# Optimization experiments

Hardware: AMD Instinct MI355X
Metric: run time of the kernel (lower is better)

Reference implementation:

```python
import jax, jax.numpy as jnp
import numpy as np

WS = (8, 8)          # window size
NHEAD = 6
D_MODEL = 192

def _rel_pos_index(ws):
    coords = np.stack(np.meshgrid(np.arange(ws[0]), np.arange(ws[1]), indexing='ij'))  # (2, wh, ww)
    cf = coords.reshape(2, -1)                          # (2, N)
    rel = cf[:, :, None] - cf[:, None, :]               # (2, N, N)
    rel = rel.transpose(1, 2, 0).astype(np.int64)       # (N, N, 2)
    rel[:, :, 0] += ws[0] - 1
    rel[:, :, 1] += ws[1] - 1
    rel[:, :, 0] *= 2 * ws[1] - 1
    return rel.sum(-1)                                  # (N, N)

REL_IDX = jnp.asarray(_rel_pos_index(WS))

def setup_inputs() -> dict:
    key = jax.random.key(0)
    ks = jax.random.split(key, 6)
    B, H, W, C = 4, 256, 256, D_MODEL
    x = jax.random.normal(ks[0], (B, H * W, C), dtype=jnp.float32)
    qkv_w = jax.random.normal(ks[1], (3 * C, C), dtype=jnp.float32) * 0.02
    qkv_b = jnp.zeros((3 * C,), dtype=jnp.float32)
    proj_w = jax.random.normal(ks[2], (C, C), dtype=jnp.float32) * 0.02
    proj_b = jnp.zeros((C,), dtype=jnp.float32)
    n_bias = (2 * WS[0] - 1) * (2 * WS[1] - 1)
    rpb_table = jax.random.normal(ks[3], (n_bias, NHEAD), dtype=jnp.float32) * 0.02
    return {"x": x, "qkv_w": qkv_w, "qkv_b": qkv_b, "proj_w": proj_w,
            "proj_b": proj_b, "rpb_table": rpb_table, "H": H, "W": W}

def reference(x, qkv_w, qkv_b, proj_w, proj_b, rpb_table, H, W):
    B, Ni, C = x.shape
    h, d = NHEAD, C // NHEAD
    wh, ww = WS
    nH, nW = H // wh, W // ww
    N = wh * ww
    # window partition: (B, H, W, C) -> (B*nH*nW, N, C)
    xw = x.reshape(B, nH, wh, nW, ww, C).transpose(0, 1, 3, 2, 4, 5).reshape(-1, N, C)
    qkv = xw @ qkv_w.T + qkv_b                           # (B_, N, 3C)
    B_ = xw.shape[0]
    qkv = qkv.reshape(B_, N, 3, h, d).transpose(2, 0, 3, 1, 4)  # (3, B_, h, N, d)
    q, k, v = qkv[0], qkv[1], qkv[2]
    scale = d ** -0.5
    attn = jnp.einsum('bhnd,bhmd->bhnm', q, k) * scale   # (B_, h, N, N)
    bias = rpb_table[REL_IDX.reshape(-1)].reshape(N, N, h).transpose(2, 0, 1)  # (h, N, N)
    attn = jax.nn.softmax(attn + bias[None], axis=-1)
    out = jnp.einsum('bhnm,bhmd->bhnd', attn, v)         # (B_, h, N, d)
    out = out.transpose(0, 2, 1, 3).reshape(B_, N, C)
    out = out @ proj_w.T + proj_b
    # window reverse: (B*nH*nW, N, C) -> (B, H*W, C)
    out = out.reshape(B, nH, nW, wh, ww, C).transpose(0, 1, 3, 2, 4, 5).reshape(B, Ni, C)
    return out
```

## Files before the change

kernel.cpp:

```cpp
#include <hip/hip_runtime.h>

#define CDIM 192
#define NHEAD 6

typedef __bf16 bf16x8 __attribute__((ext_vector_type(8)));
typedef float f32x4 __attribute__((ext_vector_type(4)));

#define Q_OFF  0
#define K_OFF  25600
#define VT_OFF 51200
#define SMEM_BYTES 78848
#define XS  200
#define QS  200
#define KS  200
#define VTS 72
#define AOS 200
#define PS  72
#define OFS 196
#define SCALE 0.17677669529663687f

__device__ __forceinline__ unsigned short f2b(float f) {
    unsigned int u = __float_as_uint(f);
    u = (u + 0x7FFFu + ((u >> 16) & 1u)) >> 16;
    return (unsigned short)u;
}

#define WS_W1   0
#define WS_W2   221184
#define WS_BIAS 294912

__global__ void prep(const float* __restrict__ qkv_w, const float* __restrict__ proj_w,
                     const float* __restrict__ rpb,
                     unsigned short* __restrict__ W1, unsigned short* __restrict__ W2,
                     float* __restrict__ BIAS) {
    int t = blockIdx.x * 256 + threadIdx.x;
    if (t < 110592) { W1[t] = f2b(qkv_w[t]); return; }
    t -= 110592;
    if (t < 36864)  { W2[t] = f2b(proj_w[t]); return; }
    t -= 36864;
    {
        int h = t >> 12, ij = t & 4095;
        int i = ij >> 6, j = ij & 63;
        int idx = ((i >> 3) - (j >> 3) + 7) * 15 + ((i & 7) - (j & 7) + 7);
        BIAS[t] = rpb[idx * NHEAD + h];
    }
}

__global__ __launch_bounds__(512)
void win_attn(const float* __restrict__ x,
              const unsigned short* __restrict__ qkv_w,
              const float* __restrict__ qkv_b,
              const unsigned short* __restrict__ proj_w,
              const float* __restrict__ proj_b,
              const float* __restrict__ bias,
              float* __restrict__ out)
{
    extern __shared__ __align__(16) char smem[];
    __bf16* ql  = (__bf16*)(smem + Q_OFF);
    __bf16* kl  = (__bf16*)(smem + K_OFF);
    __bf16* vt  = (__bf16*)(smem + VT_OFF);
    __bf16* xk  = (__bf16*)(smem + K_OFF);
    __bf16* aob = (__bf16*)(smem + K_OFF);
    float* stagef = (float*)(smem);

    const int tid  = threadIdx.x;
    const int wv   = tid >> 6;
    const int lane = tid & 63;
    const int l15  = lane & 15;
    const int g    = lane >> 4;
    const int g4   = g << 2;
    const int g8   = g << 3;

    const int wid = blockIdx.x;
    const int b   = wid >> 10;
    const int wy  = (wid >> 5) & 31;
    const int wx  = wid & 31;
    const long long base0 = (long long)(b * 65536 + wy * 8 * 256 + wx * 8) * CDIM;

    #pragma unroll
    for (int r = 0; r < 6; ++r) {
        int i = tid + r * 512;
        int t = i / 48, part = i - t * 48;
        int iy = t >> 3, ix = t & 7;
        f32x4 v = *(const f32x4*)(x + base0 + (iy * 256 + ix) * CDIM + part * 4);
        __bf16* dst = xk + t * XS + part * 4;
        dst[0] = (__bf16)v[0]; dst[1] = (__bf16)v[1];
        dst[2] = (__bf16)v[2]; dst[3] = (__bf16)v[3];
    }
    __syncthreads();

    {
        const int qstart_lut[8] = {0, 5, 10, 15, 20, 25, 30, 31};
        const int start = qstart_lut[wv];

        f32x4 acc[4][5];
        #pragma unroll
        for (int mt = 0; mt < 4; ++mt)
            #pragma unroll
            for (int jn = 0; jn < 5; ++jn)
                acc[mt][jn] = (f32x4){0.f, 0.f, 0.f, 0.f};

        #pragma unroll
        for (int kk = 0; kk < 6; ++kk) {
            bf16x8 aa[4];
            #pragma unroll
            for (int mt = 0; mt < 4; ++mt)
                aa[mt] = *(const bf16x8*)(xk + (mt * 16 + l15) * XS + kk * 32 + g8);
            #pragma unroll
            for (int jn = 0; jn < 5; ++jn) {
                int o = (start + jn) * 16 + l15;
                bf16x8 bw = *(const bf16x8*)((const __bf16*)qkv_w + o * CDIM + kk * 32 + g8);
                #pragma unroll
                for (int mt = 0; mt < 4; ++mt)
                    acc[mt][jn] = __builtin_amdgcn_mfma_f32_16x16x32_bf16(aa[mt], bw, acc[mt][jn], 0, 0, 0);
            }
        }
        __syncthreads();

        #pragma unroll
        for (int jn = 0; jn < 5; ++jn) {
            int nt = start + jn;
            int o  = nt * 16 + l15;
            float qb = qkv_b[o];
            #pragma unroll
            for (int mt = 0; mt < 4; ++mt) {
                #pragma unroll
                for (int rr = 0; rr < 4; ++rr) {
                    int tr = mt * 16 + g4 + rr;
                    float val = acc[mt][jn][rr] + qb;
                    if (nt < 12)       ql[tr * QS + o] = (__bf16)val;
                    else if (nt < 24)  kl[tr * KS + (o - 192)] = (__bf16)val;
                    else               vt[(o - 384) * VTS + tr] = (__bf16)val;
                }
            }
        }
    }
    __syncthreads();

    f32x4 sh[3][4];
    #pragma unroll
    for (int u = 0; u < 3; ++u) {
        int gu = wv * 3 + u;
        int hu = gu >> 2;
        int rb = gu & 3;

        bf16x8 aq = *(const bf16x8*)(ql + (rb * 16 + l15) * QS + hu * 32 + g8);
        #pragma unroll
        for (int ni = 0; ni < 4; ++ni) {
            bf16x8 bk = *(const bf16x8*)(kl + (ni * 16 + l15) * KS + hu * 32 + g8);
            sh[u][ni] = __builtin_amdgcn_mfma_f32_16x16x32_bf16(aq, bk, (f32x4){0.f, 0.f, 0.f, 0.f}, 0, 0, 0);
        }

        const float* brow = bias + hu * 4096;
        #pragma unroll
        for (int rr = 0; rr < 4; ++rr) {
            int row = rb * 16 + g4 + rr;
            float v0 = sh[u][0][rr] * SCALE + brow[row * 64 +  0 + l15];
            float v1 = sh[u][1][rr] * SCALE + brow[row * 64 + 16 + l15];
            float v2 = sh[u][2][rr] * SCALE + brow[row * 64 + 32 + l15];
            float v3 = sh[u][3][rr] * SCALE + brow[row * 64 + 48 + l15];
            float m = fmaxf(fmaxf(v0, v1), fmaxf(v2, v3));
            m = fmaxf(m, __shfl_xor(m, 1));
            m = fmaxf(m, __shfl_xor(m, 2));
            m = fmaxf(m, __shfl_xor(m, 4));
            m = fmaxf(m, __shfl_xor(m, 8));
            v0 = __expf(v0 - m); v1 = __expf(v1 - m);
            v2 = __expf(v2 - m); v3 = __expf(v3 - m);
            float s = v0 + v1 + v2 + v3;
            s += __shfl_xor(s, 1); s += __shfl_xor(s, 2);
            s += __shfl_xor(s, 4); s += __shfl_xor(s, 8);
            float inv = 1.0f / s;
            sh[u][0][rr] = v0 * inv;
            sh[u][1][rr] = v1 * inv;
            sh[u][2][rr] = v2 * inv;
            sh[u][3][rr] = v3 * inv;
        }
    }
    __syncthreads();

    #pragma unroll
    for (int u = 0; u < 3; ++u) {
        int gu = wv * 3 + u;
        int hu = gu >> 2;
        int rb = gu & 3;
        __bf16* ph = (__bf16*)(smem + Q_OFF) + wv * (16 * PS);

        #pragma unroll
        for (int rr = 0; rr < 4; ++rr) {
            int pr = (g4 + rr) * PS;
            ph[pr +  0 + l15] = (__bf16)sh[u][0][rr];
            ph[pr + 16 + l15] = (__bf16)sh[u][1][rr];
            ph[pr + 32 + l15] = (__bf16)sh[u][2][rr];
            ph[pr + 48 + l15] = (__bf16)sh[u][3][rr];
        }
        __threadfence_block();

        f32x4 oacc[2];
        oacc[0] = (f32x4){0.f, 0.f, 0.f, 0.f};
        oacc[1] = (f32x4){0.f, 0.f, 0.f, 0.f};
        #pragma unroll
        for (int kk = 0; kk < 2; ++kk) {
            bf16x8 pa = *(const bf16x8*)(ph + l15 * PS + kk * 32 + g8);
            #pragma unroll
            for (int nj = 0; nj < 2; ++nj) {
                bf16x8 bv = *(const bf16x8*)(vt + (hu * 32 + nj * 16 + l15) * VTS + kk * 32 + g8);
                oacc[nj] = __builtin_amdgcn_mfma_f32_16x16x32_bf16(pa, bv, oacc[nj], 0, 0, 0);
            }
        }
        __threadfence_block();
        #pragma unroll
        for (int nj = 0; nj < 2; ++nj)
            #pragma unroll
            for (int rr = 0; rr < 4; ++rr)
                aob[(rb * 16 + g4 + rr) * AOS + hu * 32 + nj * 16 + l15] = (__bf16)oacc[nj][rr];
    }
    __syncthreads();

    {
        const int pstart_lut[8] = {0, 2, 4, 6, 8, 10, 10, 10};
        const int start = pstart_lut[wv];

        f32x4 pacc[4][2];
        #pragma unroll
        for (int mt = 0; mt < 4; ++mt)
            #pragma unroll
            for (int jn = 0; jn < 2; ++jn)
                pacc[mt][jn] = (f32x4){0.f, 0.f, 0.f, 0.f};

        #pragma unroll
        for (int kk = 0; kk < 6; ++kk) {
            bf16x8 aa[4];
            #pragma unroll
            for (int mt = 0; mt < 4; ++mt)
                aa[mt] = *(const bf16x8*)(aob + (mt * 16 + l15) * AOS + kk * 32 + g8);
            #pragma unroll
            for (int jn = 0; jn < 2; ++jn) {
                int o = (start + jn) * 16 + l15;
                bf16x8 bw = *(const bf16x8*)((const __bf16*)proj_w + o * CDIM + kk * 32 + g8);
                #pragma unroll
                for (int mt = 0; mt < 4; ++mt)
                    pacc[mt][jn] = __builtin_amdgcn_mfma_f32_16x16x32_bf16(aa[mt], bw, pacc[mt][jn], 0, 0, 0);
            }
        }
        __syncthreads();
        #pragma unroll
        for (int jn = 0; jn < 2; ++jn) {
            int o = (start + jn) * 16 + l15;
            float pb = proj_b[o];
            #pragma unroll
            for (int mt = 0; mt < 4; ++mt)
                #pragma unroll
                for (int rr = 0; rr < 4; ++rr) {
                    int tr = mt * 16 + g4 + rr;
                    stagef[tr * OFS + o] = pacc[mt][jn][rr] + pb;
                }
        }
    }
    __syncthreads();

    #pragma unroll
    for (int r = 0; r < 6; ++r) {
        int i = tid + r * 512;
        int t = i / 48, part = i - t * 48;
        int iy = t >> 3, ix = t & 7;
        *(f32x4*)(out + base0 + (iy * 256 + ix) * CDIM + part * 4) =
            *(const f32x4*)(stagef + t * OFS + part * 4);
    }
}

extern "C" void kernel_launch(void* const* d_in, const int* in_sizes, int n_in,
                              void* d_out, int out_size, void* d_ws, size_t ws_size,
                              hipStream_t stream) {
    const float* x      = (const float*)d_in[0];
    const float* qkv_w  = (const float*)d_in[1];
    const float* qkv_b  = (const float*)d_in[2];
    const float* proj_w = (const float*)d_in[3];
    const float* proj_b = (const float*)d_in[4];
    const float* rpb    = (const float*)d_in[5];
    float* outp = (float*)d_out;

    char* ws = (char*)d_ws;
    unsigned short* W1 = (unsigned short*)(ws + WS_W1);
    unsigned short* W2 = (unsigned short*)(ws + WS_W2);
    float* BIAS = (float*)(ws + WS_BIAS);

    hipFuncSetAttribute((const void*)win_attn,
                        hipFuncAttributeMaxDynamicSharedMemorySize, SMEM_BYTES);

    prep<<<672, 256, 0, stream>>>(qkv_w, proj_w, rpb, W1, W2, BIAS);
    win_attn<<<4096, 512, SMEM_BYTES, stream>>>(x, W1, qkv_b, W2, proj_b, BIAS, outp);
}
```

Before: 392.8 us.

## Load x fragments directly from global into MFMA registers, skipping LDS staging

The QKV projection now reads x straight from global memory into MFMA A-operand registers and converts to bf16 in registers. This removes the shared-memory staging copy and one barrier. The M dimension is split into two passes of two row tiles each, which shrinks the accumulator set. Launch bounds now request 4 blocks per CU (512, 4) to cap register use. Each of the 8 waves re-reads the same x rows from global or L2 instead of sharing one LDS copy, and the per-lane 16-byte loads are strided by rows, so memory traffic may rise.

After: 518.7 us. +32.1%, slower.

```diff
diff --git a/kernel.cpp b/kernel.cpp
--- a/kernel.cpp
+++ b/kernel.cpp
@@ -10,7 +10,6 @@
 #define K_OFF  25600
 #define VT_OFF 51200
 #define SMEM_BYTES 78848
-#define XS  200
 #define QS  200
 #define KS  200
 #define VTS 72
@@ -23,6 +22,13 @@
     unsigned int u = __float_as_uint(f);
     u = (u + 0x7FFFu + ((u >> 16) & 1u)) >> 16;
     return (unsigned short)u;
+}
+
+__device__ __forceinline__ bf16x8 cvt8(f32x4 a, f32x4 b) {
+    bf16x8 r;
+    r[0] = (__bf16)a[0]; r[1] = (__bf16)a[1]; r[2] = (__bf16)a[2]; r[3] = (__bf16)a[3];
+    r[4] = (__bf16)b[0]; r[5] = (__bf16)b[1]; r[6] = (__bf16)b[2]; r[7] = (__bf16)b[3];
+    return r;
 }
 
 #define WS_W1   0
@@ -46,7 +52,7 @@
     }
 }
 
-__global__ __launch_bounds__(512)
+__global__ __launch_bounds__(512, 4)
 void win_attn(const float* __restrict__ x,
               const unsigned short* __restrict__ qkv_w,
               const float* __restrict__ qkv_b,
@@ -59,7 +65,6 @@
     __bf16* ql  = (__bf16*)(smem + Q_OFF);
     __bf16* kl  = (__bf16*)(smem + K_OFF);
     __bf16* vt  = (__bf16*)(smem + VT_OFF);
-    __bf16* xk  = (__bf16*)(smem + K_OFF);
     __bf16* aob = (__bf16*)(smem + K_OFF);
     float* stagef = (float*)(smem);
 
@@ -77,60 +82,59 @@
     const int wx  = wid & 31;
     const long long base0 = (long long)(b * 65536 + wy * 8 * 256 + wx * 8) * CDIM;
 
-    #pragma unroll
-    for (int r = 0; r < 6; ++r) {
-        int i = tid + r * 512;
-        int t = i / 48, part = i - t * 48;
-        int iy = t >> 3, ix = t & 7;
-        f32x4 v = *(const f32x4*)(x + base0 + (iy * 256 + ix) * CDIM + part * 4);
-        __bf16* dst = xk + t * XS + part * 4;
-        dst[0] = (__bf16)v[0]; dst[1] = (__bf16)v[1];
-        dst[2] = (__bf16)v[2]; dst[3] = (__bf16)v[3];
-    }
-    __syncthreads();
-
     {
         const int qstart_lut[8] = {0, 5, 10, 15, 20, 25, 30, 31};
         const int start = qstart_lut[wv];
 
-        f32x4 acc[4][5];
-        #pragma unroll
-        for (int mt = 0; mt < 4; ++mt)
-            #pragma unroll
-            for (int jn = 0; jn < 5; ++jn)
-                acc[mt][jn] = (f32x4){0.f, 0.f, 0.f, 0.f};
-
-        #pragma unroll
-        for (int kk = 0; kk < 6; ++kk) {
-            bf16x8 aa[4];
-            #pragma unroll
-            for (int mt = 0; mt < 4; ++mt)
-                aa[mt] = *(const bf16x8*)(xk + (mt * 16 + l15) * XS + kk * 32 + g8);
+        #pragma unroll
+        for (int pass = 0; pass < 2; ++pass) {
+            const float* xr[2];
+            #pragma unroll
+            for (int im = 0; im < 2; ++im) {
+                int t0 = (pass * 2 + im) * 16 + l15;
+                xr[im] = x + base0 + ((t0 >> 3) * 256 + (t0 & 7)) * CDIM;
+            }
+
+            f32x4 acc[2][5];
+            #pragma unroll
+            for (int im = 0; im < 2; ++im)
+                #pragma unroll
+                for (int jn = 0; jn < 5; ++jn)
+                    acc[im][jn] = (f32x4){0.f, 0.f, 0.f, 0.f};
+
+            #pragma unroll
+            for (int kk = 0; kk < 6; ++kk) {
+                bf16x8 aa[2];
+                #pragma unroll
+                for (int im = 0; im < 2; ++im) {
+                    f32x4 lo = *(const f32x4*)(xr[im] + kk * 32 + g8);
+                    f32x4 hi = *(const f32x4*)(xr[im] + kk * 32 + g8 + 4);
+                    aa[im] = cvt8(lo, hi);
+                }
+                #pragma unroll
+                for (int jn = 0; jn < 5; ++jn) {
+                    int o = (start + jn) * 16 + l15;
+                    bf16x8 bw = *(const bf16x8*)((const __bf16*)qkv_w + o * CDIM + kk * 32 + g8);
+                    #pragma unroll
+                    for (int im = 0; im < 2; ++im)
+                        acc[im][jn] = __builtin_amdgcn_mfma_f32_16x16x32_bf16(aa[im], bw, acc[im][jn], 0, 0, 0);
+                }
+            }
             #pragma unroll
             for (int jn = 0; jn < 5; ++jn) {
-                int o = (start + jn) * 16 + l15;
-                bf16x8 bw = *(const bf16x8*)((const __bf16*)qkv_w + o * CDIM + kk * 32 + g8);
-                #pragma unroll
-                for (int mt = 0; mt < 4; ++mt)
-                    acc[mt][jn] = __builtin_amdgcn_mfma_f32_16x16x32_bf16(aa[mt], bw, acc[mt][jn], 0, 0, 0);
-            }
-        }
-        __syncthreads();
-
-        #pragma unroll
-        for (int jn = 0; jn < 5; ++jn) {
-            int nt = start + jn;
-            int o  = nt * 16 + l15;
-            float qb = qkv_b[o];
-            #pragma unroll
-            for (int mt = 0; mt < 4; ++mt) {
-                #pragma unroll
-                for (int rr = 0; rr < 4; ++rr) {
-                    int tr = mt * 16 + g4 + rr;
-                    float val = acc[mt][jn][rr] + qb;
-                    if (nt < 12)       ql[tr * QS + o] = (__bf16)val;
-                    else if (nt < 24)  kl[tr * KS + (o - 192)] = (__bf16)val;
-                    else               vt[(o - 384) * VTS + tr] = (__bf16)val;
+                int nt = start + jn;
+                int o  = nt * 16 + l15;
+                float qb = qkv_b[o];
+                #pragma unroll
+                for (int im = 0; im < 2; ++im) {
+                    #pragma unroll
+                    for (int rr = 0; rr < 4; ++rr) {
+                        int tr = (pass * 2 + im) * 16 + g4 + rr;
+                        float val = acc[im][jn][rr] + qb;
+                        if (nt < 12)       ql[tr * QS + o] = (__bf16)val;
+                        else if (nt < 24)  kl[tr * KS + (o - 192)] = (__bf16)val;
+                        else               vt[(o - 384) * VTS + tr] = (__bf16)val;
+                    }
                 }
             }
         }
```

## Process two windows per block to reuse weight fragments across windows

Applied to the files above, without the earlier changes.

Each block now handles two attention windows, with separate LDS halves for each. Weight fragments for the QKV and output projections are loaded once per k-step and applied to both windows, halving global weight traffic per window. This doubles LDS use and accumulator registers, which reduces occupancy and risks register spills.

Result: faster. 371.7 us (-5.4%).

```diff
diff --git a/kernel.cpp b/kernel.cpp
--- a/kernel.cpp
+++ b/kernel.cpp
@@ -6,10 +6,11 @@
 typedef __bf16 bf16x8 __attribute__((ext_vector_type(8)));
 typedef float f32x4 __attribute__((ext_vector_type(4)));
 
+#define HB     78848
 #define Q_OFF  0
 #define K_OFF  25600
 #define VT_OFF 51200
-#define SMEM_BYTES 78848
+#define SMEM_BYTES (2 * HB)
 #define XS  200
 #define QS  200
 #define KS  200
@@ -56,12 +57,6 @@
               float* __restrict__ out)
 {
     extern __shared__ __align__(16) char smem[];
-    __bf16* ql  = (__bf16*)(smem + Q_OFF);
-    __bf16* kl  = (__bf16*)(smem + K_OFF);
-    __bf16* vt  = (__bf16*)(smem + VT_OFF);
-    __bf16* xk  = (__bf16*)(smem + K_OFF);
-    __bf16* aob = (__bf16*)(smem + K_OFF);
-    float* stagef = (float*)(smem);
 
     const int tid  = threadIdx.x;
     const int wv   = tid >> 6;
@@ -71,21 +66,29 @@
     const int g4   = g << 2;
     const int g8   = g << 3;
 
-    const int wid = blockIdx.x;
-    const int b   = wid >> 10;
-    const int wy  = (wid >> 5) & 31;
-    const int wx  = wid & 31;
-    const long long base0 = (long long)(b * 65536 + wy * 8 * 256 + wx * 8) * CDIM;
-
-    #pragma unroll
-    for (int r = 0; r < 6; ++r) {
-        int i = tid + r * 512;
-        int t = i / 48, part = i - t * 48;
-        int iy = t >> 3, ix = t & 7;
-        f32x4 v = *(const f32x4*)(x + base0 + (iy * 256 + ix) * CDIM + part * 4);
-        __bf16* dst = xk + t * XS + part * 4;
-        dst[0] = (__bf16)v[0]; dst[1] = (__bf16)v[1];
-        dst[2] = (__bf16)v[2]; dst[3] = (__bf16)v[3];
+    long long base[2];
+    #pragma unroll
+    for (int w = 0; w < 2; ++w) {
+        int wid = blockIdx.x * 2 + w;
+        int b   = wid >> 10;
+        int wy  = (wid >> 5) & 31;
+        int wx  = wid & 31;
+        base[w] = (long long)(b * 65536 + wy * 8 * 256 + wx * 8) * CDIM;
+    }
+
+    #pragma unroll
+    for (int w = 0; w < 2; ++w) {
+        __bf16* xk = (__bf16*)(smem + w * HB + K_OFF);
+        #pragma unroll
+        for (int r = 0; r < 6; ++r) {
+            int i = tid + r * 512;
+            int t = i / 48, part = i - t * 48;
+            int iy = t >> 3, ix = t & 7;
+            f32x4 v = *(const f32x4*)(x + base[w] + (iy * 256 + ix) * CDIM + part * 4);
+            __bf16* dst = xk + t * XS + part * 4;
+            dst[0] = (__bf16)v[0]; dst[1] = (__bf16)v[1];
+            dst[2] = (__bf16)v[2]; dst[3] = (__bf16)v[3];
+        }
     }
     __syncthreads();
 
@@ -93,26 +96,35 @@
         const int qstart_lut[8] = {0, 5, 10, 15, 20, 25, 30, 31};
         const int start = qstart_lut[wv];
 
-        f32x4 acc[4][5];
-        #pragma unroll
-        for (int mt = 0; mt < 4; ++mt)
-            #pragma unroll
-            for (int jn = 0; jn < 5; ++jn)
-                acc[mt][jn] = (f32x4){0.f, 0.f, 0.f, 0.f};
+        f32x4 acc[2][4][5];
+        #pragma unroll
+        for (int w = 0; w < 2; ++w)
+            #pragma unroll
+            for (int mt = 0; mt < 4; ++mt)
+                #pragma unroll
+                for (int jn = 0; jn < 5; ++jn)
+                    acc[w][mt][jn] = (f32x4){0.f, 0.f, 0.f, 0.f};
 
         #pragma unroll
         for (int kk = 0; kk < 6; ++kk) {
-            bf16x8 aa[4];
-            #pragma unroll
-            for (int mt = 0; mt < 4; ++mt)
-                aa[mt] = *(const bf16x8*)(xk + (mt * 16 + l15) * XS + kk * 32 + g8);
+            bf16x8 bw[5];
             #pragma unroll
             for (int jn = 0; jn < 5; ++jn) {
                 int o = (start + jn) * 16 + l15;
-                bf16x8 bw = *(const bf16x8*)((const __bf16*)qkv_w + o * CDIM + kk * 32 + g8);
+                bw[jn] = *(const bf16x8*)((const __bf16*)qkv_w + o * CDIM + kk * 32 + g8);
+            }
+            #pragma unroll
+            for (int w = 0; w < 2; ++w) {
+                const __bf16* xk = (const __bf16*)(smem + w * HB + K_OFF);
+                bf16x8 aa[4];
                 #pragma unroll
                 for (int mt = 0; mt < 4; ++mt)
-                    acc[mt][jn] = __builtin_amdgcn_mfma_f32_16x16x32_bf16(aa[mt], bw, acc[mt][jn], 0, 0, 0);
+                    aa[mt] = *(const bf16x8*)(xk + (mt * 16 + l15) * XS + kk * 32 + g8);
+                #pragma unroll
+                for (int jn = 0; jn < 5; ++jn)
+                    #pragma unroll
+                    for (int mt = 0; mt < 4; ++mt)
+                        acc[w][mt][jn] = __builtin_amdgcn_mfma_f32_16x16x32_bf16(aa[mt], bw[jn], acc[w][mt][jn], 0, 0, 0);
             }
         }
         __syncthreads();
@@ -123,96 +135,112 @@
             int o  = nt * 16 + l15;
             float qb = qkv_b[o];
             #pragma unroll
-            for (int mt = 0; mt < 4; ++mt) {
-                #pragma unroll
-                for (int rr = 0; rr < 4; ++rr) {
-                    int tr = mt * 16 + g4 + rr;
-                    float val = acc[mt][jn][rr] + qb;
-                    if (nt < 12)       ql[tr * QS + o] = (__bf16)val;
-                    else if (nt < 24)  kl[tr * KS + (o - 192)] = (__bf16)val;
-                    else               vt[(o - 384) * VTS + tr] = (__bf16)val;
+            for (int w = 0; w < 2; ++w) {
+                __bf16* ql  = (__bf16*)(smem + w * HB + Q_OFF);
+                __bf16* kl  = (__bf16*)(smem + w * HB + K_OFF);
+                __bf16* vtw = (__bf16*)(smem + w * HB + VT_OFF);
+                #pragma unroll
+                for (int mt = 0; mt < 4; ++mt) {
+                    #pragma unroll
+                    for (int rr = 0; rr < 4; ++rr) {
+                        int tr = mt * 16 + g4 + rr;
+                        float val = acc[w][mt][jn][rr] + qb;
+                        if (nt < 12)       ql[tr * QS + o] = (__bf16)val;
+                        else if (nt < 24)  kl[tr * KS + (o - 192)] = (__bf16)val;
+                        else               vtw[(o - 384) * VTS + tr] = (__bf16)val;
+                    }
                 }
             }
         }
     }
     __syncthreads();
 
-    f32x4 sh[3][4];
-    #pragma unroll
-    for (int u = 0; u < 3; ++u) {
-        int gu = wv * 3 + u;
-        int hu = gu >> 2;
-        int rb = gu & 3;
-
-        bf16x8 aq = *(const bf16x8*)(ql + (rb * 16 + l15) * QS + hu * 32 + g8);
-        #pragma unroll
-        for (int ni = 0; ni < 4; ++ni) {
-            bf16x8 bk = *(const bf16x8*)(kl + (ni * 16 + l15) * KS + hu * 32 + g8);
-            sh[u][ni] = __builtin_amdgcn_mfma_f32_16x16x32_bf16(aq, bk, (f32x4){0.f, 0.f, 0.f, 0.f}, 0, 0, 0);
-        }
-
-        const float* brow = bias + hu * 4096;
-        #pragma unroll
-        for (int rr = 0; rr < 4; ++rr) {
-            int row = rb * 16 + g4 + rr;
-            float v0 = sh[u][0][rr] * SCALE + brow[row * 64 +  0 + l15];
-            float v1 = sh[u][1][rr] * SCALE + brow[row * 64 + 16 + l15];
-            float v2 = sh[u][2][rr] * SCALE + brow[row * 64 + 32 + l15];
-            float v3 = sh[u][3][rr] * SCALE + brow[row * 64 + 48 + l15];
-            float m = fmaxf(fmaxf(v0, v1), fmaxf(v2, v3));
-            m = fmaxf(m, __shfl_xor(m, 1));
-            m = fmaxf(m, __shfl_xor(m, 2));
-            m = fmaxf(m, __shfl_xor(m, 4));
-            m = fmaxf(m, __shfl_xor(m, 8));
-            v0 = __expf(v0 - m); v1 = __expf(v1 - m);
-            v2 = __expf(v2 - m); v3 = __expf(v3 - m);
-            float s = v0 + v1 + v2 + v3;
-            s += __shfl_xor(s, 1); s += __shfl_xor(s, 2);
-            s += __shfl_xor(s, 4); s += __shfl_xor(s, 8);
-            float inv = 1.0f / s;
-            sh[u][0][rr] = v0 * inv;
-            sh[u][1][rr] = v1 * inv;
-            sh[u][2][rr] = v2 * inv;
-            sh[u][3][rr] = v3 * inv;
-        }
-    }
-    __syncthreads();
-
-    #pragma unroll
-    for (int u = 0; u < 3; ++u) {
-        int gu = wv * 3 + u;
-        int hu = gu >> 2;
-        int rb = gu & 3;
-        __bf16* ph = (__bf16*)(smem + Q_OFF) + wv * (16 * PS);
-
-        #pragma unroll
-        for (int rr = 0; rr < 4; ++rr) {
-            int pr = (g4 + rr) * PS;
-            ph[pr +  0 + l15] = (__bf16)sh[u][0][rr];
-            ph[pr + 16 + l15] = (__bf16)sh[u][1][rr];
-            ph[pr + 32 + l15] = (__bf16)sh[u][2][rr];
-            ph[pr + 48 + l15] = (__bf16)sh[u][3][rr];
-        }
-        __threadfence_block();
-
-        f32x4 oacc[2];
-        oacc[0] = (f32x4){0.f, 0.f, 0.f, 0.f};
-        oacc[1] = (f32x4){0.f, 0.f, 0.f, 0.f};
-        #pragma unroll
-        for (int kk = 0; kk < 2; ++kk) {
-            bf16x8 pa = *(const bf16x8*)(ph + l15 * PS + kk * 32 + g8);
-            #pragma unroll
-            for (int nj = 0; nj < 2; ++nj) {
-                bf16x8 bv = *(const bf16x8*)(vt + (hu * 32 + nj * 16 + l15) * VTS + kk * 32 + g8);
-                oacc[nj] = __builtin_amdgcn_mfma_f32_16x16x32_bf16(pa, bv, oacc[nj], 0, 0, 0);
-            }
-        }
-        __threadfence_block();
-        #pragma unroll
-        for (int nj = 0; nj < 2; ++nj)
-            #pragma unroll
-            for (int rr = 0; rr < 4; ++rr)
-                aob[(rb * 16 + g4 + rr) * AOS + hu * 32 + nj * 16 + l15] = (__bf16)oacc[nj][rr];
+    f32x4 sh[2][3][4];
+    #pragma unroll
+    for (int w = 0; w < 2; ++w) {
+        const __bf16* ql = (const __bf16*)(smem + w * HB + Q_OFF);
+        const __bf16* kl = (const __bf16*)(smem + w * HB + K_OFF);
+        #pragma unroll
+        for (int u = 0; u < 3; ++u) {
+            int gu = wv * 3 + u;
+            int hu = gu >> 2;
+            int rb = gu & 3;
+
+            bf16x8 aq = *(const bf16x8*)(ql + (rb * 16 + l15) * QS + hu * 32 + g8);
+            #pragma unroll
+            for (int ni = 0; ni < 4; ++ni) {
+                bf16x8 bk = *(const bf16x8*)(kl + (ni * 16 + l15) * KS + hu * 32 + g8);
+                sh[w][u][ni] = __builtin_amdgcn_mfma_f32_16x16x32_bf16(aq, bk, (f32x4){0.f, 0.f, 0.f, 0.f}, 0, 0, 0);
+            }
+
+            const float* brow = bias + hu * 4096;
+            #pragma unroll
+            for (int rr = 0; rr < 4; ++rr) {
+                int row = rb * 16 + g4 + rr;
+                float v0 = sh[w][u][0][rr] * SCALE + brow[row * 64 +  0 + l15];
+                float v1 = sh[w][u][1][rr] * SCALE + brow[row * 64 + 16 + l15];
+                float v2 = sh[w][u][2][rr] * SCALE + brow[row * 64 + 32 + l15];
+                float v3 = sh[w][u][3][rr] * SCALE + brow[row * 64 + 48 + l15];
+                float m = fmaxf(fmaxf(v0, v1), fmaxf(v2, v3));
+                m = fmaxf(m, __shfl_xor(m, 1));
+                m = fmaxf(m, __shfl_xor(m, 2));
+                m = fmaxf(m, __shfl_xor(m, 4));
+                m = fmaxf(m, __shfl_xor(m, 8));
+                v0 = __expf(v0 - m); v1 = __expf(v1 - m);
+                v2 = __expf(v2 - m); v3 = __expf(v3 - m);
+                float s = v0 + v1 + v2 + v3;
+                s += __shfl_xor(s, 1); s += __shfl_xor(s, 2);
+                s += __shfl_xor(s, 4); s += __shfl_xor(s, 8);
+                float inv = 1.0f / s;
+                sh[w][u][0][rr] = v0 * inv;
+                sh[w][u][1][rr] = v1 * inv;
+                sh[w][u][2][rr] = v2 * inv;
+                sh[w][u][3][rr] = v3 * inv;
+            }
+        }
+    }
+    __syncthreads();
+
+    #pragma unroll
+    for (int w = 0; w < 2; ++w) {
+        __bf16* ph  = (__bf16*)(smem + w * HB + Q_OFF) + wv * (16 * PS);
+        const __bf16* vtw = (const __bf16*)(smem + w * HB + VT_OFF);
+        __bf16* aob = (__bf16*)(smem + w * HB + K_OFF);
+        #pragma unroll
+        for (int u = 0; u < 3; ++u) {
+            int gu = wv * 3 + u;
+            int hu = gu >> 2;
+            int rb = gu & 3;
+
+            #pragma unroll
+            for (int rr = 0; rr < 4; ++rr) {
+                int pr = (g4 + rr) * PS;
+                ph[pr +  0 + l15] = (__bf16)sh[w][u][0][rr];
+                ph[pr + 16 + l15] = (__bf16)sh[w][u][1][rr];
+                ph[pr + 32 + l15] = (__bf16)sh[w][u][2][rr];
+                ph[pr + 48 + l15] = (__bf16)sh[w][u][3][rr];
+            }
+            __threadfence_block();
+
+            f32x4 oacc[2];
+            oacc[0] = (f32x4){0.f, 0.f, 0.f, 0.f};
+            oacc[1] = (f32x4){0.f, 0.f, 0.f, 0.f};
+            #pragma unroll
+            for (int kk = 0; kk < 2; ++kk) {
+                bf16x8 pa = *(const bf16x8*)(ph + l15 * PS + kk * 32 + g8);
+                #pragma unroll
+                for (int nj = 0; nj < 2; ++nj) {
+                    bf16x8 bv = *(const bf16x8*)(vtw + (hu * 32 + nj * 16 + l15) * VTS + kk * 32 + g8);
+                    oacc[nj] = __builtin_amdgcn_mfma_f32_16x16x32_bf16(pa, bv, oacc[nj], 0, 0, 0);
+                }
+            }
+            __threadfence_block();
+            #pragma unroll
+            for (int nj = 0; nj < 2; ++nj)
+                #pragma unroll
+                for (int rr = 0; rr < 4; ++rr)
+                    aob[(rb * 16 + g4 + rr) * AOS + hu * 32 + nj * 16 + l15] = (__bf16)oacc[nj][rr];
+        }
     }
     __syncthreads();
 
@@ -220,51 +248,69 @@
         const int pstart_lut[8] = {0, 2, 4, 6, 8, 10, 10, 10};
         const int start = pstart_lut[wv];
 
-        f32x4 pacc[4][2];
-        #pragma unroll
-        for (int mt = 0; mt < 4; ++mt)
-            #pragma unroll
-            for (int jn = 0; jn < 2; ++jn)
-                pacc[mt][jn] = (f32x4){0.f, 0.f, 0.f, 0.f};
+        f32x4 pacc[2][4][2];
+        #pragma unroll
+        for (int w = 0; w < 2; ++w)
+            #pragma unroll
+            for (int mt = 0; mt < 4; ++mt)
+                #pragma unroll
+                for (int jn = 0; jn < 2; ++jn)
+                    pacc[w][mt][jn] = (f32x4){0.f, 0.f, 0.f, 0.f};
 
         #pragma unroll
         for (int kk = 0; kk < 6; ++kk) {
-            bf16x8 aa[4];
-            #pragma unroll
-            for (int mt = 0; mt < 4; ++mt)
-                aa[mt] = *(const bf16x8*)(aob + (mt * 16 + l15) * AOS + kk * 32 + g8);
+            bf16x8 bw[2];
             #pragma unroll
             for (int jn = 0; jn < 2; ++jn) {
                 int o = (start + jn) * 16 + l15;
-                bf16x8 bw = *(const bf16x8*)((const __bf16*)proj_w + o * CDIM + kk * 32 + g8);
+                bw[jn] = *(const bf16x8*)((const __bf16*)proj_w + o * CDIM + kk * 32 + g8);
+            }
+            #pragma unroll
+            for (int w = 0; w < 2; ++w) {
+                const __bf16* aob = (const __bf16*)(smem + w * HB + K_OFF);
+                bf16x8 aa[4];
                 #pragma unroll
                 for (int mt = 0; mt < 4; ++mt)
-                    pacc[mt][jn] = __builtin_amdgcn_mfma_f32_16x16x32_bf16(aa[mt], bw, pacc[mt][jn], 0, 0, 0);
+                    aa[mt] = *(const bf16x8*)(aob + (mt * 16 + l15) * AOS + kk * 32 + g8);
+                #pragma unroll
+                for (int jn = 0; jn < 2; ++jn)
+                    #pragma unroll
+                    for (int mt = 0; mt < 4; ++mt)
+                        pacc[w][mt][jn] = __builtin_amdgcn_mfma_f32_16x16x32_bf16(aa[mt], bw[jn], pacc[w][mt][jn], 0, 0, 0);
             }
         }
         __syncthreads();
+
         #pragma unroll
         for (int jn = 0; jn < 2; ++jn) {
             int o = (start + jn) * 16 + l15;
             float pb = proj_b[o];
             #pragma unroll
-            for (int mt = 0; mt < 4; ++mt)
-                #pragma unroll
-                for (int rr = 0; rr < 4; ++rr) {
-                    int tr = mt * 16 + g4 + rr;
-                    stagef[tr * OFS + o] = pacc[mt][jn][rr] + pb;
-                }
-        }
-    }
-    __syncthreads();
-
-    #pragma unroll
-    for (int r = 0; r < 6; ++r) {
-        int i = tid + r * 512;
-        int t = i / 48, part = i - t * 48;
-        int iy = t >> 3, ix = t & 7;
-        *(f32x4*)(out + base0 + (iy * 256 + ix) * CDIM + part * 4) =
-            *(const f32x4*)(stagef + t * OFS + part * 4);
+            for (int w = 0; w < 2; ++w) {
+                float* stagef = (float*)(smem + w * HB);
+                #pragma unroll
+                for (int mt = 0; mt < 4; ++mt)
+                    #pragma unroll
+                    for (int rr = 0; rr < 4; ++rr) {
+                        int tr = mt * 16 + g4 + rr;
+                        stagef[tr * OFS + o] = pacc[w][mt][jn][rr] + pb;
+                    }
+            }
+        }
+    }
+    __syncthreads();
+
+    #pragma unroll
+    for (int w = 0; w < 2; ++w) {
+        const float* stagef = (const float*)(smem + w * HB);
+        #pragma unroll
+        for (int r = 0; r < 6; ++r) {
+            int i = tid + r * 512;
+            int t = i / 48, part = i - t * 48;
+            int iy = t >> 3, ix = t & 7;
+            *(f32x4*)(out + base[w] + (iy * 256 + ix) * CDIM + part * 4) =
+                *(const f32x4*)(stagef + t * OFS + part * 4);
+        }
     }
 }
 
@@ -288,5 +334,5 @@
                         hipFuncAttributeMaxDynamicSharedMemorySize, SMEM_BYTES);
 
     prep<<<672, 256, 0, stream>>>(qkv_w, proj_w, rpb, W1, W2, BIAS);
-    win_attn<<<4096, 512, SMEM_BYTES, stream>>>(x, W1, qkv_b, W2, proj_b, BIAS, outp);
+    win_attn<<<2048, 512, SMEM_BYTES, stream>>>(x, W1, qkv_b, W2, proj_b, BIAS, outp);
 }
```

## Process two windows per 1024-thread block with split shared memory halves

Applied to the files above, without the earlier changes.

Each block now handles two windows with two independent 512-thread groups, each using its own half of a doubled LDS allocation, and the grid is halved. The x-to-bf16 staging store is also vectorised into a single 8-byte write via manual rounding. The intent is to reduce per-block launch overhead and let one workgroup hold two windows' worth of work. The cost is that the two windows are coupled by block-wide barriers, the 1024-thread launch bound can force tighter register limits and spills, and the 157KB LDS request may limit residency per CU.

Result: slower. 432.3 us (+10.1%).

```diff
diff --git a/kernel.cpp b/kernel.cpp
--- a/kernel.cpp
+++ b/kernel.cpp
@@ -5,11 +5,13 @@
 
 typedef __bf16 bf16x8 __attribute__((ext_vector_type(8)));
 typedef float f32x4 __attribute__((ext_vector_type(4)));
-
+typedef unsigned short u16x4 __attribute__((ext_vector_type(4)));
+
+#define HB     78848
 #define Q_OFF  0
 #define K_OFF  25600
 #define VT_OFF 51200
-#define SMEM_BYTES 78848
+#define SMEM_BYTES (2 * HB)
 #define XS  200
 #define QS  200
 #define KS  200
@@ -46,7 +48,7 @@
     }
 }
 
-__global__ __launch_bounds__(512)
+__global__ __launch_bounds__(1024)
 void win_attn(const float* __restrict__ x,
               const unsigned short* __restrict__ qkv_w,
               const float* __restrict__ qkv_b,
@@ -56,43 +58,47 @@
               float* __restrict__ out)
 {
     extern __shared__ __align__(16) char smem[];
-    __bf16* ql  = (__bf16*)(smem + Q_OFF);
-    __bf16* kl  = (__bf16*)(smem + K_OFF);
-    __bf16* vt  = (__bf16*)(smem + VT_OFF);
-    __bf16* xk  = (__bf16*)(smem + K_OFF);
-    __bf16* aob = (__bf16*)(smem + K_OFF);
-    float* stagef = (float*)(smem);
-
-    const int tid  = threadIdx.x;
-    const int wv   = tid >> 6;
-    const int lane = tid & 63;
-    const int l15  = lane & 15;
-    const int g    = lane >> 4;
-    const int g4   = g << 2;
-    const int g8   = g << 3;
-
-    const int wid = blockIdx.x;
+
+    const int tid   = threadIdx.x;
+    const int wv    = tid >> 6;
+    const int wg    = wv >> 3;
+    const int wvin  = wv & 7;
+    const int tidin = tid & 511;
+    const int lane  = tid & 63;
+    const int l15   = lane & 15;
+    const int g     = lane >> 4;
+    const int g4    = g << 2;
+    const int g8    = g << 3;
+
+    const int wid = blockIdx.x * 2 + wg;
     const int b   = wid >> 10;
     const int wy  = (wid >> 5) & 31;
     const int wx  = wid & 31;
-    const long long base0 = (long long)(b * 65536 + wy * 8 * 256 + wx * 8) * CDIM;
+    const long long base = (long long)(b * 65536 + wy * 8 * 256 + wx * 8) * CDIM;
+
+    char* half = smem + wg * HB;
+    __bf16* ql  = (__bf16*)(half + Q_OFF);
+    __bf16* kl  = (__bf16*)(half + K_OFF);
+    __bf16* vtw = (__bf16*)(half + VT_OFF);
+
+    const int qstart_lut[8] = {0, 5, 10, 15, 20, 25, 30, 31};
+    const int pstart_lut[8] = {0, 2, 4, 6, 8, 10, 10, 10};
+    const int qstart = qstart_lut[wvin];
+    const int pstart = pstart_lut[wvin];
 
     #pragma unroll
     for (int r = 0; r < 6; ++r) {
-        int i = tid + r * 512;
+        int i = tidin + r * 512;
         int t = i / 48, part = i - t * 48;
         int iy = t >> 3, ix = t & 7;
-        f32x4 v = *(const f32x4*)(x + base0 + (iy * 256 + ix) * CDIM + part * 4);
-        __bf16* dst = xk + t * XS + part * 4;
-        dst[0] = (__bf16)v[0]; dst[1] = (__bf16)v[1];
-        dst[2] = (__bf16)v[2]; dst[3] = (__bf16)v[3];
-    }
-    __syncthreads();
-
-    {
-        const int qstart_lut[8] = {0, 5, 10, 15, 20, 25, 30, 31};
-        const int start = qstart_lut[wv];
-
+        f32x4 v = *(const f32x4*)(x + base + (iy * 256 + ix) * CDIM + part * 4);
+        u16x4 h;
+        h[0] = f2b(v[0]); h[1] = f2b(v[1]); h[2] = f2b(v[2]); h[3] = f2b(v[3]);
+        *(u16x4*)(kl + t * XS + part * 4) = h;
+    }
+    __syncthreads();
+
+    {
         f32x4 acc[4][5];
         #pragma unroll
         for (int mt = 0; mt < 4; ++mt)
@@ -105,10 +111,10 @@
             bf16x8 aa[4];
             #pragma unroll
             for (int mt = 0; mt < 4; ++mt)
-                aa[mt] = *(const bf16x8*)(xk + (mt * 16 + l15) * XS + kk * 32 + g8);
+                aa[mt] = *(const bf16x8*)(kl + (mt * 16 + l15) * XS + kk * 32 + g8);
             #pragma unroll
             for (int jn = 0; jn < 5; ++jn) {
-                int o = (start + jn) * 16 + l15;
+                int o = (qstart + jn) * 16 + l15;
                 bf16x8 bw = *(const bf16x8*)((const __bf16*)qkv_w + o * CDIM + kk * 32 + g8);
                 #pragma unroll
                 for (int mt = 0; mt < 4; ++mt)
@@ -119,7 +125,7 @@
 
         #pragma unroll
         for (int jn = 0; jn < 5; ++jn) {
-            int nt = start + jn;
+            int nt = qstart + jn;
             int o  = nt * 16 + l15;
             float qb = qkv_b[o];
             #pragma unroll
@@ -130,7 +136,7 @@
                     float val = acc[mt][jn][rr] + qb;
                     if (nt < 12)       ql[tr * QS + o] = (__bf16)val;
                     else if (nt < 24)  kl[tr * KS + (o - 192)] = (__bf16)val;
-                    else               vt[(o - 384) * VTS + tr] = (__bf16)val;
+                    else               vtw[(o - 384) * VTS + tr] = (__bf16)val;
                 }
             }
         }
@@ -140,7 +146,7 @@
     f32x4 sh[3][4];
     #pragma unroll
     for (int u = 0; u < 3; ++u) {
-        int gu = wv * 3 + u;
+        int gu = wvin * 3 + u;
         int hu = gu >> 2;
         int rb = gu & 3;
 
@@ -178,48 +184,48 @@
     }
     __syncthreads();
 
-    #pragma unroll
-    for (int u = 0; u < 3; ++u) {
-        int gu = wv * 3 + u;
-        int hu = gu >> 2;
-        int rb = gu & 3;
-        __bf16* ph = (__bf16*)(smem + Q_OFF) + wv * (16 * PS);
-
-        #pragma unroll
-        for (int rr = 0; rr < 4; ++rr) {
-            int pr = (g4 + rr) * PS;
-            ph[pr +  0 + l15] = (__bf16)sh[u][0][rr];
-            ph[pr + 16 + l15] = (__bf16)sh[u][1][rr];
-            ph[pr + 32 + l15] = (__bf16)sh[u][2][rr];
-            ph[pr + 48 + l15] = (__bf16)sh[u][3][rr];
-        }
-        __threadfence_block();
-
-        f32x4 oacc[2];
-        oacc[0] = (f32x4){0.f, 0.f, 0.f, 0.f};
-        oacc[1] = (f32x4){0.f, 0.f, 0.f, 0.f};
-        #pragma unroll
-        for (int kk = 0; kk < 2; ++kk) {
-            bf16x8 pa = *(const bf16x8*)(ph + l15 * PS + kk * 32 + g8);
-            #pragma unroll
-            for (int nj = 0; nj < 2; ++nj) {
-                bf16x8 bv = *(const bf16x8*)(vt + (hu * 32 + nj * 16 + l15) * VTS + kk * 32 + g8);
-                oacc[nj] = __builtin_amdgcn_mfma_f32_16x16x32_bf16(pa, bv, oacc[nj], 0, 0, 0);
-            }
-        }
-        __threadfence_block();
-        #pragma unroll
-        for (int nj = 0; nj < 2; ++nj)
-            #pragma unroll
-            for (int rr = 0; rr < 4; ++rr)
-                aob[(rb * 16 + g4 + rr) * AOS + hu * 32 + nj * 16 + l15] = (__bf16)oacc[nj][rr];
-    }
-    __syncthreads();
-
-    {
-        const int pstart_lut[8] = {0, 2, 4, 6, 8, 10, 10, 10};
-        const int start = pstart_lut[wv];
-
+    {
+        __bf16* ph  = ql + wvin * (16 * PS);
+        __bf16* aob = kl;
+        #pragma unroll
+        for (int u = 0; u < 3; ++u) {
+            int gu = wvin * 3 + u;
+            int hu = gu >> 2;
+            int rb = gu & 3;
+
+            #pragma unroll
+            for (int rr = 0; rr < 4; ++rr) {
+                int pr = (g4 + rr) * PS;
+                ph[pr +  0 + l15] = (__bf16)sh[u][0][rr];
+                ph[pr + 16 + l15] = (__bf16)sh[u][1][rr];
+                ph[pr + 32 + l15] = (__bf16)sh[u][2][rr];
+                ph[pr + 48 + l15] = (__bf16)sh[u][3][rr];
+            }
+            __threadfence_block();
+
+            f32x4 oacc[2];
+            oacc[0] = (f32x4){0.f, 0.f, 0.f, 0.f};
+            oacc[1] = (f32x4){0.f, 0.f, 0.f, 0.f};
+            #pragma unroll
+            for (int kk = 0; kk < 2; ++kk) {
+                bf16x8 pa = *(const bf16x8*)(ph + l15 * PS + kk * 32 + g8);
+                #pragma unroll
+                for (int nj = 0; nj < 2; ++nj) {
+                    bf16x8 bv = *(const bf16x8*)(vtw + (hu * 32 + nj * 16 + l15) * VTS + kk * 32 + g8);
+                    oacc[nj] = __builtin_amdgcn_mfma_f32_16x16x32_bf16(pa, bv, oacc[nj], 0, 0, 0);
+                }
+            }
+            __threadfence_block();
+            #pragma unroll
+            for (int nj = 0; nj < 2; ++nj)
+                #pragma unroll
+                for (int rr = 0; rr < 4; ++rr)
+                    aob[(rb * 16 + g4 + rr) * AOS + hu * 32 + nj * 16 + l15] = (__bf16)oacc[nj][rr];
+        }
+    }
+    __syncthreads();
+
+    {
         f32x4 pacc[4][2];
         #pragma unroll
         for (int mt = 0; mt < 4; ++mt)
@@ -227,6 +233,7 @@
             for (int jn = 0; jn < 2; ++jn)
                 pacc[mt][jn] = (f32x4){0.f, 0.f, 0.f, 0.f};
 
+        const __bf16* aob = kl;
         #pragma unroll
         for (int kk = 0; kk < 6; ++kk) {
             bf16x8 aa[4];
@@ -235,7 +242,7 @@
                 aa[mt] = *(const bf16x8*)(aob + (mt * 16 + l15) * AOS + kk * 32 + g8);
             #pragma unroll
             for (int jn = 0; jn < 2; ++jn) {
-                int o = (start + jn) * 16 + l15;
+                int o = (pstart + jn) * 16 + l15;
                 bf16x8 bw = *(const bf16x8*)((const __bf16*)proj_w + o * CDIM + kk * 32 + g8);
                 #pragma unroll
                 for (int mt = 0; mt < 4; ++mt)
@@ -243,9 +250,11 @@
             }
         }
         __syncthreads();
+
+        float* stagef = (float*)half;
         #pragma unroll
         for (int jn = 0; jn < 2; ++jn) {
-            int o = (start + jn) * 16 + l15;
+            int o = (pstart + jn) * 16 + l15;
             float pb = proj_b[o];
             #pragma unroll
             for (int mt = 0; mt < 4; ++mt)
@@ -258,13 +267,16 @@
     }
     __syncthreads();
 
-    #pragma unroll
-    for (int r = 0; r < 6; ++r) {
-        int i = tid + r * 512;
-        int t = i / 48, part = i - t * 48;
-        int iy = t >> 3, ix = t & 7;
-        *(f32x4*)(out + base0 + (iy * 256 + ix) * CDIM + part * 4) =
-            *(const f32x4*)(stagef + t * OFS + part * 4);
+    {
+        const float* stagef = (const float*)half;
+        #pragma unroll
+        for (int r = 0; r < 6; ++r) {
+            int i = tidin + r * 512;
+            int t = i / 48, part = i - t * 48;
+            int iy = t >> 3, ix = t & 7;
+            *(f32x4*)(out + base + (iy * 256 + ix) * CDIM + part * 4) =
+                *(const f32x4*)(stagef + t * OFS + part * 4);
+        }
     }
 }
 
@@ -288,5 +300,5 @@
                         hipFuncAttributeMaxDynamicSharedMemorySize, SMEM_BYTES);
 
     prep<<<672, 256, 0, stream>>>(qkv_w, proj_w, rpb, W1, W2, BIAS);
-    win_attn<<<4096, 512, SMEM_BYTES, stream>>>(x, W1, qkv_b, W2, proj_b, BIAS, outp);
+    win_attn<<<2048, 1024, SMEM_BYTES, stream>>>(x, W1, qkv_b, W2, proj_b, BIAS, outp);
 }
```
